# Optimization experiments

Measured on AMD Instinct MI355X. Metric: run time of the kernel, lower is better.

## Reference

```python
import jax, jax.numpy as jnp
import numpy as np

NUM_HEAD = 16
MASKED_BIAS = -10000.0


def setup_inputs() -> dict:
    key = jax.random.key(0)
    k1, k2, k3 = jax.random.split(key, 3)
    B, M, N = 2, 2048, 1024
    x = jax.random.normal(k1, (B, M, N), dtype=jnp.float32)
    w_attn = jax.random.normal(k2, (N, 3 * N), dtype=jnp.float32) * 0.02
    w_proj = jax.random.normal(k3, (N, N), dtype=jnp.float32) * 0.02
    b_attn = jnp.zeros((3 * N,), dtype=jnp.float32)
    b_proj = jnp.zeros((N,), dtype=jnp.float32)
    return {"x": x, "w_attn": w_attn, "w_proj": w_proj,
            "b_attn": b_attn, "b_proj": b_proj}


def reference(x, w_attn, w_proj, b_attn, b_proj):
    B, M, N = x.shape
    H = NUM_HEAD
    d = N // H  # head dim
    # fused QKV projection: [B,M,3N]
    qkv = jnp.einsum('bmn,nd->bmd', x, w_attn) + b_attn
    q, k, v = jnp.split(qkv, 3, axis=-1)
    # split heads -> [B,H,M,d]
    q = q.reshape(B, M, H, d).transpose(0, 2, 1, 3)
    k = k.reshape(B, M, H, d).transpose(0, 2, 1, 3)
    v = v.reshape(B, M, H, d).transpose(0, 2, 1, 3)
    # scaled dot-product scores [B,H,M,M]
    scores = jnp.einsum('bhqd,bhkd->bhqk', q, k) / jnp.sqrt(jnp.float32(d))
    causal = jnp.tril(jnp.ones((M, M), dtype=bool))  # GPT-2 bias buffer
    scores = jnp.where(causal, scores, jnp.float32(MASKED_BIAS))
    attn = jax.nn.softmax(scores, axis=-1)
    # context [B,H,M,d] -> [B,M,N]
    ctx = jnp.einsum('bhqk,bhkd->bhqd', attn, v)
    ctx = ctx.transpose(0, 2, 1, 3).reshape(B, M, N)
    # output projection
    out = jnp.einsum('bmn,no->bmo', ctx, w_proj) + b_proj
    return out
```

## Files before the change

kernel.cpp:

```cpp
#include <hip/hip_runtime.h>

typedef __attribute__((ext_vector_type(8))) __bf16 bf16x8;
typedef __attribute__((ext_vector_type(4))) __bf16 bf16x4;
typedef __attribute__((ext_vector_type(4))) float f32x4;

__device__ __forceinline__ void async_copy16(const void* g, void* l) {
    __builtin_amdgcn_global_load_lds(
        (const __attribute__((address_space(1))) void*)g,
        (__attribute__((address_space(3))) void*)l, 16, 0, 0);
}

__global__ __launch_bounds__(256) void prep_k(
    const float* __restrict__ x, __bf16* __restrict__ xb,
    const float* __restrict__ wa, __bf16* __restrict__ wAt,
    const float* __restrict__ wp, __bf16* __restrict__ wPt)
{
    __shared__ float tile[32][33];
    const int bx = blockIdx.x;
    if (bx < 2048) {
        size_t i = ((size_t)bx * 256 + threadIdx.x) * 8;
        float4 a = *(const float4*)&x[i];
        float4 b = *(const float4*)&x[i + 4];
        bf16x8 o;
        o[0] = (__bf16)a.x; o[1] = (__bf16)a.y; o[2] = (__bf16)a.z; o[3] = (__bf16)a.w;
        o[4] = (__bf16)b.x; o[5] = (__bf16)b.y; o[6] = (__bf16)b.z; o[7] = (__bf16)b.w;
        *(bf16x8*)&xb[i] = o;
        return;
    }
    const float* src; __bf16* dst; int R, C, c0, r0;
    if (bx < 5120) {
        int id = bx - 2048;
        src = wa; dst = wAt; R = 1024; C = 3072;
        c0 = (id % 96) * 32; r0 = (id / 96) * 32;
    } else {
        int id = bx - 5120;
        src = wp; dst = wPt; R = 1024; C = 1024;
        c0 = (id & 31) * 32; r0 = (id >> 5) * 32;
    }
    int tx = threadIdx.x & 31, ty = threadIdx.x >> 5;
    for (int i = ty; i < 32; i += 8)
        tile[i][tx] = src[(size_t)(r0 + i) * C + (c0 + tx)];
    __syncthreads();
    for (int i = ty; i < 32; i += 8)
        dst[(size_t)(c0 + i) * R + (r0 + tx)] = (__bf16)tile[tx][i];
}

template <int MODE, int TN>
__global__ __launch_bounds__(256) void gemm_bt(
    const __bf16* __restrict__ A, const __bf16* __restrict__ Bt,
    const float* __restrict__ bias, int K,
    __bf16* __restrict__ O0, __bf16* __restrict__ O1, __bf16* __restrict__ O2,
    float* __restrict__ Of)
{
    constexpr int NJ = TN / 32;
    __shared__ __align__(16) __bf16 lds_a[2][128 * 32];
    __shared__ __align__(16) __bf16 lds_b[2][TN * 32];
    const int row0 = blockIdx.x * 128;
    const int col0 = blockIdx.y * TN;
    const int tid  = threadIdx.x;
    const int lane = tid & 63;
    const int w    = tid >> 6;
    const int wm   = (w >> 1) * 64, wn = (w & 1) * (TN / 2);
    const int quad = lane >> 4, l16 = lane & 15;

    auto stage = [&](int pb, int kb) {
#pragma unroll
        for (int t = 0; t < 2; ++t) {
            int s = t * 256 + tid;
            int L = s >> 3, c = (s & 7) ^ (L & 7);
            int row = 2 * L + (c >> 2), ch = c & 3;
            async_copy16(&A[(size_t)(row0 + row) * K + kb + ch * 8],
                         (char*)&lds_a[pb][0] + (t * 256 + w * 64) * 16);
        }
#pragma unroll
        for (int t = 0; t < TN / 64; ++t) {
            int s = t * 256 + tid;
            int L = s >> 3, c = (s & 7) ^ (L & 7);
            int row = 2 * L + (c >> 2), ch = c & 3;
            async_copy16(&Bt[(size_t)(col0 + row) * K + kb + ch * 8],
                         (char*)&lds_b[pb][0] + (t * 256 + w * 64) * 16);
        }
    };

    const int nIter = K >> 5;
    f32x4 acc[4][NJ] = {};
    stage(0, 0);
    for (int it = 0; it < nIter; ++it) {
        __syncthreads();
        if (it + 1 < nIter) stage((it + 1) & 1, (it + 1) << 5);
        const __bf16* la = &lds_a[it & 1][0];
        const __bf16* lb = &lds_b[it & 1][0];
        bf16x8 af[4], bfr[NJ];
#pragma unroll
        for (int i = 0; i < 4; ++i) {
            int r = wm + i * 16 + l16;
            int L = r >> 1, g = ((r & 1) * 4 + quad) ^ (L & 7);
            af[i] = *(const bf16x8*)&la[L * 64 + g * 8];
        }
#pragma unroll
        for (int j = 0; j < NJ; ++j) {
            int r = wn + j * 16 + l16;
            int L = r >> 1, g = ((r & 1) * 4 + quad) ^ (L & 7);
            bfr[j] = *(const bf16x8*)&lb[L * 64 + g * 8];
        }
#pragma unroll
        for (int i = 0; i < 4; ++i)
#pragma unroll
            for (int j = 0; j < NJ; ++j)
                acc[i][j] = __builtin_amdgcn_mfma_f32_16x16x32_bf16(
                    af[i], bfr[j], acc[i][j], 0, 0, 0);
    }

#pragma unroll
    for (int i = 0; i < 4; ++i) {
        int grow = row0 + wm + i * 16 + quad * 4;
#pragma unroll
        for (int j = 0; j < NJ; ++j) {
            int gcol = col0 + wn + j * 16 + l16;
            float bv = bias[gcol];
            if constexpr (MODE == 0) {
                int which = gcol >> 10;
                int n  = gcol & 1023;
                int hh = n >> 6, dd = n & 63;
                int bb = grow >> 11, mm0 = grow & 2047;
                int bhh = bb * 16 + hh;
                if (which == 2) {
                    int w64 = mm0 & 63;
                    int mi = (mm0 & ~63) | (w64 & 32) | ((w64 & 12) << 1)
                             | ((w64 & 16) >> 2);
                    bf16x4 pk;
#pragma unroll
                    for (int r = 0; r < 4; ++r)
                        pk[r] = (__bf16)(acc[i][j][r] + bv);
                    *(bf16x4*)&O2[((size_t)bhh * 64 + dd) * 2048 + mi] = pk;
                } else {
#pragma unroll
                    for (int r = 0; r < 4; ++r) {
                        float v = acc[i][j][r] + bv;
                        if (which == 0)
                            O0[((size_t)bhh * 2048 + mm0 + r) * 64 + dd] =
                                (__bf16)(v * 0.18033688011112042f);
                        else
                            O1[((size_t)bhh * 2048 + mm0 + r) * 64 + dd] =
                                (__bf16)v;
                    }
                }
            } else {
#pragma unroll
                for (int r = 0; r < 4; ++r) {
                    int gr = grow + r;
                    Of[(size_t)gr * 1024 + gcol] = acc[i][j][r] + bv;
                }
            }
        }
    }
}

__global__ __launch_bounds__(256) void attn_kernel(
    const __bf16* __restrict__ Qh, const __bf16* __restrict__ Kh,
    const __bf16* __restrict__ Vt, __bf16* __restrict__ ctx)
{
    const int M = 2048, D = 64;
    const int bh = blockIdx.x;
    const int qt = 31 - blockIdx.y;
    const int b = bh >> 4, h = bh & 15;
    const int tid = threadIdx.x, lane = tid & 63, w = tid >> 6;
    const int quad = lane >> 4, l16 = lane & 15;

    const int q0 = qt * 64;
    const int nIter = qt + 1;

    __shared__ __align__(16) __bf16 lds_k[2][64 * 64];
    __shared__ __align__(16) __bf16 lds_v[2][64 * 64];

    const __bf16* Qp = Qh + (size_t)bh * M * D;
    const __bf16* Kp = Kh + (size_t)bh * M * D;
    const __bf16* Vp = Vt + (size_t)bh * D * M;

    const int qw = q0 + w * 16;

    bf16x8 qf[2];
#pragma unroll
    for (int c = 0; c < 2; ++c)
        qf[c] = *(const bf16x8*)
            &Qp[(size_t)(qw + l16) * D + c * 32 + quad * 8];

    f32x4 acc2[4] = {};
    f32x4 acc_s = {};
    const __bf16 onev = (__bf16)1.0f;
    const bf16x8 ones8 = {onev, onev, onev, onev, onev, onev, onev, onev};

    auto stage = [&](int pb, int kb) {
#pragma unroll
        for (int t = 0; t < 2; ++t) {
            int c = w * 128 + t * 64 + lane;
            int row = c >> 3, ch = c & 7;
            int gch = ch ^ (row & 7);
            async_copy16(&Kp[(size_t)(kb + row) * 64 + gch * 8],
                         (char*)&lds_k[pb][0] + (w * 128 + t * 64) * 16);
            async_copy16(&Vp[(size_t)row * M + kb + gch * 8],
                         (char*)&lds_v[pb][0] + (w * 128 + t * 64) * 16);
        }
    };

    stage(0, 0);

    for (int it = 0; it < nIter; ++it) {
        const int kb = it << 6;
        __syncthreads();
        if (it + 1 < nIter) stage((it + 1) & 1, kb + 64);
        const __bf16* kt = &lds_k[it & 1][0];
        const __bf16* vt = &lds_v[it & 1][0];

        f32x4 s[4];
#pragma unroll
        for (int t = 0; t < 4; ++t) {
            f32x4 tt = {};
#pragma unroll
            for (int c = 0; c < 2; ++c) {
                int ch = ((c << 2) + quad) ^ (l16 & 7);
                bf16x8 kf = *(const bf16x8*)
                    &kt[(((t << 4) + l16) << 6) + (ch << 3)];
                tt = __builtin_amdgcn_mfma_f32_16x16x32_bf16(
                    kf, qf[c], tt, 0, 0, 0);
            }
            s[t] = tt;
        }
        if (kb + 63 > qw) {
#pragma unroll
            for (int t = 0; t < 4; ++t)
#pragma unroll
                for (int r = 0; r < 4; ++r)
                    if (kb + t * 16 + quad * 4 + r > qw + l16)
                        s[t][r] = -1e30f;
        }
        bf16x8 pf32[2];
#pragma unroll
        for (int tp = 0; tp < 2; ++tp) {
            bf16x8 pp;
#pragma unroll
            for (int r = 0; r < 4; ++r) {
                pp[r]     = (__bf16)exp2f(s[2 * tp][r]);
                pp[4 + r] = (__bf16)exp2f(s[2 * tp + 1][r]);
            }
            pf32[tp] = pp;
        }
#pragma unroll
        for (int f = 0; f < 4; ++f) {
            int row = (f << 4) + l16;
#pragma unroll
            for (int tp = 0; tp < 2; ++tp) {
                int g = ((tp << 2) + quad) ^ (row & 7);
                bf16x8 vv = *(const bf16x8*)&vt[(row << 6) + (g << 3)];
                acc2[f] = __builtin_amdgcn_mfma_f32_16x16x32_bf16(
                    vv, pf32[tp], acc2[f], 0, 0, 0);
            }
        }
#pragma unroll
        for (int tp = 0; tp < 2; ++tp)
            acc_s = __builtin_amdgcn_mfma_f32_16x16x32_bf16(
                ones8, pf32[tp], acc_s, 0, 0, 0);
    }

    __syncthreads();
    __bf16* ldsT = &lds_k[0][0];
    const float l = acc_s[0];
#pragma unroll
    for (int f = 0; f < 4; ++f) {
        bf16x4 ov;
#pragma unroll
        for (int r = 0; r < 4; ++r)
            ov[r] = (__bf16)(acc2[f][r] / l);
        *(bf16x4*)&ldsT[(w * 16 + l16) * 72 + f * 16 + quad * 4] = ov;
    }
    __syncthreads();
    {
        int qq = tid >> 2;
        int dp = (tid & 3) * 16;
        const __bf16* src = &ldsT[qq * 72 + dp];
        __bf16* dst = &ctx[((size_t)(b * 2048 + q0 + qq)) * 1024 + h * 64 + dp];
        *(bf16x8*)&dst[0] = *(const bf16x8*)&src[0];
        *(bf16x8*)&dst[8] = *(const bf16x8*)&src[8];
    }
}

extern "C" void kernel_launch(void* const* d_in, const int* in_sizes, int n_in,
                              void* d_out, int out_size, void* d_ws, size_t ws_size,
                              hipStream_t stream) {
    const float* x      = (const float*)d_in[0];
    const float* w_attn = (const float*)d_in[1];
    const float* w_proj = (const float*)d_in[2];
    const float* b_attn = (const float*)d_in[3];
    const float* b_proj = (const float*)d_in[4];
    float* out = (float*)d_out;

    char* ws = (char*)d_ws;
    __bf16* xb  = (__bf16*)(ws);
    __bf16* ctx = (__bf16*)(ws);
    __bf16* wAt = (__bf16*)(ws + 8388608);
    __bf16* wPt = (__bf16*)(ws + 14680064);
    __bf16* Vt  = (__bf16*)(ws + 16777216);
    __bf16* Qh  = (__bf16*)d_out;
    __bf16* Kh  = (__bf16*)d_out + 4194304;

    prep_k<<<6144, 256, 0, stream>>>(x, xb, w_attn, wAt, w_proj, wPt);
    gemm_bt<0, 128><<<dim3(32, 24), 256, 0, stream>>>(xb, wAt, b_attn, 1024,
                                                      Qh, Kh, Vt, nullptr);
    attn_kernel<<<dim3(32, 32), 256, 0, stream>>>(Qh, Kh, Vt, ctx);
    gemm_bt<1, 64><<<dim3(32, 16), 256, 0, stream>>>(ctx, wPt, b_proj, 1024,
                                                     nullptr, nullptr, nullptr, out);
}
```

Baseline: 175.4 us.

## Use 128-row query tiles with 8 waves sharing K/V staging in attention

```diff
diff --git a/kernel.cpp b/kernel.cpp
--- a/kernel.cpp
+++ b/kernel.cpp
@@ -156,22 +156,21 @@
     }
 }
 
-__global__ __launch_bounds__(256) void attn_kernel(
+__global__ __launch_bounds__(512, 4) void attn_kernel(
     const __bf16* __restrict__ Qh, const __bf16* __restrict__ Kh,
     const __bf16* __restrict__ Vt, __bf16* __restrict__ ctx)
 {
     const int M = 2048, D = 64;
     const int bh = blockIdx.x;
-    const int qt = 31 - blockIdx.y;
+    const int qt = 15 - blockIdx.y;
     const int b = bh >> 4, h = bh & 15;
     const int tid = threadIdx.x, lane = tid & 63, w = tid >> 6;
     const int quad = lane >> 4, l16 = lane & 15;
 
-    const int q0 = qt * 64;
-    const int nIter = qt + 1;
-
-    __shared__ __align__(16) __bf16 lds_k[2][64 * 64];
-    __shared__ __align__(16) __bf16 lds_v[2][64 * 64];
+    const int q0 = qt * 128;
+    const int nIter = 2 * qt + 2;
+
+    __shared__ __align__(16) __bf16 smem[2][2][64 * 64];
 
     const __bf16* Qp = Qh + (size_t)bh * M * D;
     const __bf16* Kp = Kh + (size_t)bh * M * D;
@@ -184,48 +183,68 @@
     for (int c = 0; c < 2; ++c)
         qf[c] = *(const bf16x8*)
             &Qp[(size_t)(qw + l16) * D + c * 32 + quad * 8];
+
+    int ko[8];
+#pragma unroll
+    for (int t = 0; t < 4; ++t)
+#pragma unroll
+        for (int c = 0; c < 2; ++c) {
+            int ch = ((c << 2) + quad) ^ (l16 & 7);
+            ko[t * 2 + c] = (((t << 4) + l16) << 6) + (ch << 3);
+        }
+    int vo[8];
+#pragma unroll
+    for (int f = 0; f < 4; ++f)
+#pragma unroll
+        for (int tp = 0; tp < 2; ++tp) {
+            int row = (f << 4) + l16;
+            int g = ((tp << 2) + quad) ^ (row & 7);
+            vo[f * 2 + tp] = (row << 6) + (g << 3);
+        }
+
+    const int cch = w * 64 + lane;
+    const int srow = cch >> 3, sch = (cch & 7) ^ (srow & 7);
+    const __bf16* kgp = &Kp[(size_t)srow * 64 + sch * 8];
+    const __bf16* vgp = &Vp[(size_t)srow * M + sch * 8];
+    char* const lbase = (char*)smem + w * 1024;
+
+    auto stage = [&](int pb) {
+        char* d = lbase + pb * 16384;
+        async_copy16(kgp, d);
+        async_copy16(vgp, d + 8192);
+        kgp += 4096;
+        vgp += 64;
+    };
 
     f32x4 acc2[4] = {};
     f32x4 acc_s = {};
     const __bf16 onev = (__bf16)1.0f;
     const bf16x8 ones8 = {onev, onev, onev, onev, onev, onev, onev, onev};
 
-    auto stage = [&](int pb, int kb) {
-#pragma unroll
-        for (int t = 0; t < 2; ++t) {
-            int c = w * 128 + t * 64 + lane;
-            int row = c >> 3, ch = c & 7;
-            int gch = ch ^ (row & 7);
-            async_copy16(&Kp[(size_t)(kb + row) * 64 + gch * 8],
-                         (char*)&lds_k[pb][0] + (w * 128 + t * 64) * 16);
-            async_copy16(&Vp[(size_t)row * M + kb + gch * 8],
-                         (char*)&lds_v[pb][0] + (w * 128 + t * 64) * 16);
-        }
-    };
-
-    stage(0, 0);
+    stage(0);
 
     for (int it = 0; it < nIter; ++it) {
         const int kb = it << 6;
         __syncthreads();
-        if (it + 1 < nIter) stage((it + 1) & 1, kb + 64);
-        const __bf16* kt = &lds_k[it & 1][0];
-        const __bf16* vt = &lds_v[it & 1][0];
+        if (it + 1 < nIter) stage((it + 1) & 1);
+        if (kb > qw + 15) continue;
+        const __bf16* kt = &smem[it & 1][0][0];
+        const __bf16* vt = &smem[it & 1][1][0];
 
         f32x4 s[4];
+        __builtin_amdgcn_s_setprio(1);
 #pragma unroll
         for (int t = 0; t < 4; ++t) {
             f32x4 tt = {};
 #pragma unroll
             for (int c = 0; c < 2; ++c) {
-                int ch = ((c << 2) + quad) ^ (l16 & 7);
-                bf16x8 kf = *(const bf16x8*)
-                    &kt[(((t << 4) + l16) << 6) + (ch << 3)];
+                bf16x8 kf = *(const bf16x8*)(kt + ko[t * 2 + c]);
                 tt = __builtin_amdgcn_mfma_f32_16x16x32_bf16(
                     kf, qf[c], tt, 0, 0, 0);
             }
             s[t] = tt;
         }
+        __builtin_amdgcn_s_setprio(0);
         if (kb + 63 > qw) {
 #pragma unroll
             for (int t = 0; t < 4; ++t)
@@ -245,13 +264,12 @@
             }
             pf32[tp] = pp;
         }
+        __builtin_amdgcn_s_setprio(1);
 #pragma unroll
         for (int f = 0; f < 4; ++f) {
-            int row = (f << 4) + l16;
 #pragma unroll
             for (int tp = 0; tp < 2; ++tp) {
-                int g = ((tp << 2) + quad) ^ (row & 7);
-                bf16x8 vv = *(const bf16x8*)&vt[(row << 6) + (g << 3)];
+                bf16x8 vv = *(const bf16x8*)(vt + vo[f * 2 + tp]);
                 acc2[f] = __builtin_amdgcn_mfma_f32_16x16x32_bf16(
                     vv, pf32[tp], acc2[f], 0, 0, 0);
             }
@@ -260,17 +278,18 @@
         for (int tp = 0; tp < 2; ++tp)
             acc_s = __builtin_amdgcn_mfma_f32_16x16x32_bf16(
                 ones8, pf32[tp], acc_s, 0, 0, 0);
+        __builtin_amdgcn_s_setprio(0);
     }
 
     __syncthreads();
-    __bf16* ldsT = &lds_k[0][0];
-    const float l = acc_s[0];
+    __bf16* ldsT = (__bf16*)smem;
+    const float rinv = 1.0f / acc_s[0];
 #pragma unroll
     for (int f = 0; f < 4; ++f) {
         bf16x4 ov;
 #pragma unroll
         for (int r = 0; r < 4; ++r)
-            ov[r] = (__bf16)(acc2[f][r] / l);
+            ov[r] = (__bf16)(acc2[f][r] * rinv);
         *(bf16x4*)&ldsT[(w * 16 + l16) * 72 + f * 16 + quad * 4] = ov;
     }
     __syncthreads();
@@ -306,7 +325,7 @@
     prep_k<<<6144, 256, 0, stream>>>(x, xb, w_attn, wAt, w_proj, wPt);
     gemm_bt<0, 128><<<dim3(32, 24), 256, 0, stream>>>(xb, wAt, b_attn, 1024,
                                                       Qh, Kh, Vt, nullptr);
-    attn_kernel<<<dim3(32, 32), 256, 0, stream>>>(Qh, Kh, Vt, ctx);
+    attn_kernel<<<dim3(32, 16), 512, 0, stream>>>(Qh, Kh, Vt, ctx);
     gemm_bt<1, 64><<<dim3(32, 16), 256, 0, stream>>>(ctx, wPt, b_proj, 1024,
                                                      nullptr, nullptr, nullptr, out);
 }
```

Result: no change. 174.3 us (-0.6%).
